# Kernel optimization log

Hardware: AMD Instinct MI355X
Metric: run time of the kernel (lower is better)

Reference implementation:

```python
import jax, jax.numpy as jnp
import numpy as np


def setup_inputs() -> dict:
    mesh = 2048
    N = mesh * mesh
    key = jax.random.key(0)
    k1, k2, k3, k4, k5 = jax.random.split(key, 5)
    theta = jax.random.normal(k1, (N - 1,), dtype=jnp.float32) * 1e-4
    phi = jax.random.normal(k2, (N - 1,), dtype=jnp.float32) * 1e-4
    psi = jax.random.normal(k3, (N - 1,), dtype=jnp.float32) * 1e-4
    state_re = jax.random.normal(k4, (N, 2, 1), dtype=jnp.float32)
    state_im = jax.random.normal(k5, (N, 2, 1), dtype=jnp.float32)
    # normalize spinors so |<s|s>| = 1 (physical states are normalized)
    norm = jnp.sqrt(jnp.sum(state_re**2 + state_im**2, axis=(1, 2), keepdims=True))
    state_re = state_re / norm
    state_im = state_im / norm
    return {"theta": theta, "phi": phi, "psi": psi,
            "state_re": state_re, "state_im": state_im}


def _deform(theta, phi, psi, state_re, state_im):
    # per-site SU(2) matrices, [N-1, 2, 2]
    ct, st = jnp.cos(theta), jnp.sin(theta)
    cp, sp = jnp.cos(phi), jnp.sin(phi)
    cq, sq = jnp.cos(psi), jnp.sin(psi)
    su_re = jnp.stack([jnp.stack([ct * cp, -st * cq], -1),
                       jnp.stack([st * cq, ct * cp], -1)], -2)  # [N-1,2,2]
    su_im = jnp.stack([jnp.stack([ct * sp, -st * sq], -1),
                       jnp.stack([-st * sq, -ct * sp], -1)], -2)
    d_re = jnp.einsum('nij,njk->nik', su_re, state_re[1:]) - \
           jnp.einsum('nij,njk->nik', su_im, state_im[1:])
    d_im = jnp.einsum('nij,njk->nik', su_re, state_im[1:]) + \
           jnp.einsum('nij,njk->nik', su_im, state_re[1:])
    def_re = jnp.concatenate([state_re[:1], d_re], axis=0)
    def_im = jnp.concatenate([state_im[:1], d_im], axis=0)
    return def_re, def_im


def _hs_distance(a_re, a_im, b_re, b_im):
    # Hilbert-Schmidt distance between 2-spinors, elementwise over leading dims
    rr = jnp.sum(a_re * b_re + a_im * b_im, axis=-1)
    ri = jnp.sum(a_re * b_im - a_im * b_re, axis=-1)
    return jnp.sqrt(jnp.abs(1.0 - rr**2 - ri**2))


def reference(theta, phi, psi, state_re, state_im):
    N = state_re.shape[0]
    mesh = int(np.sqrt(N))
    def_re, def_im = _deform(theta, phi, psi, state_re, state_im)
    # [mesh, mesh, 2] grids
    g_re = def_re.reshape(mesh, mesh, 2)
    g_im = def_im.reshape(mesh, mesh, 2)
    # v: neighbor at (i, j+1) with wrap; h: (i+1, j); d: (i+1, j+1)
    v = _hs_distance(g_re, g_im,
                     jnp.roll(g_re, -1, axis=1), jnp.roll(g_im, -1, axis=1))
    h = _hs_distance(g_re, g_im,
                     jnp.roll(g_re, -1, axis=0), jnp.roll(g_im, -1, axis=0))
    d = _hs_distance(g_re, g_im,
                     jnp.roll(jnp.roll(g_re, -1, axis=0), -1, axis=1),
                     jnp.roll(jnp.roll(g_im, -1, axis=0), -1, axis=1))
    return jnp.stack([v, h, d])  # [3, mesh, mesh]
```

## Files before the change

kernel.cpp:

```cpp
#include <hip/hip_runtime.h>
#include <math.h>

#define TILE  32
#define HALO  33
#define NHALO (HALO * HALO)
#define NGRP  9
#define NASSIGN (HALO * NGRP)
#define TPB   512

__device__ __forceinline__ float4 deform1(float th, float ph, float ps,
                                          float2 r, float2 im, bool origin) {
    float st, ct, sp, cp, sq, cq;
    __sincosf(th, &st, &ct);
    __sincosf(ph, &sp, &cp);
    __sincosf(ps, &sq, &cq);
    float a = ct * cp;
    float b = st * cq;
    float c = ct * sp;
    float d = st * sq;
    float4 d4;
    d4.x = a * r.x - b * r.y - c * im.x + d * im.y;
    d4.y = b * r.x + a * r.y + d * im.x + c * im.y;
    d4.z = a * im.x - b * im.y + c * r.x - d * r.y;
    d4.w = b * im.x + a * im.y - d * r.x - c * r.y;
    if (origin) d4 = make_float4(r.x, r.y, im.x, im.y);
    return d4;
}

__device__ __forceinline__ float hsdist(float4 A, float4 B) {
    float rr = A.x * B.x + A.y * B.y + A.z * B.z + A.w * B.w;
    float ri = A.x * B.z + A.y * B.w - A.z * B.x - A.w * B.y;
    return sqrtf(fabsf(1.0f - rr * rr - ri * ri));
}

__global__ __launch_bounds__(TPB, 4) void qwz_deform_dirichlet_kernel(
    const float* __restrict__ theta,
    const float* __restrict__ phi,
    const float* __restrict__ psi,
    const float2* __restrict__ sre,
    const float2* __restrict__ sim,
    float* __restrict__ out,
    int mesh)
{
    const int N = mesh * mesh;
    __shared__ float4 tile[NHALO];

    const int tid  = threadIdx.x;
    const int lane = tid & 63;
    const int bi = blockIdx.y * TILE;
    const int bj = blockIdx.x * TILE;

    if (tid < NASSIGN) {
        const int r = tid / NGRP;
        const int g = tid - r * NGRP;
        int gi = bi + r; if (gi >= mesh) gi -= mesh;
        const bool colwrap = (bj + 4 * g >= mesh);
        int gcol = bj + 4 * g; if (colwrap) gcol -= mesh;
        const int n0 = gi * mesh + gcol;

        float4 thq, phq, psq;
        if (n0 + 4 < N) {
            thq = *(const float4*)(theta + n0);
            phq = *(const float4*)(phi   + n0);
            psq = *(const float4*)(psi   + n0);
        } else {
            thq = make_float4(theta[n0], theta[n0 + 1], theta[n0 + 2], 0.f);
            phq = make_float4(phi[n0],   phi[n0 + 1],   phi[n0 + 2],   0.f);
            psq = make_float4(psi[n0],   psi[n0 + 1],   psi[n0 + 2],   0.f);
        }
        const float4 s01 = *(const float4*)((const float*)sre + 2 * n0);
        const float4 s23 = *(const float4*)((const float*)sre + 2 * n0 + 4);
        const float4 i01 = *(const float4*)((const float*)sim + 2 * n0);
        const float4 i23 = *(const float4*)((const float*)sim + 2 * n0 + 4);

        float thm = __shfl_up(thq.w, 1, 64);
        float phm = __shfl_up(phq.w, 1, 64);
        float psm = __shfl_up(psq.w, 1, 64);
        if (lane == 0 || g == 0 || colwrap) {
            int am = (n0 > 0) ? n0 - 1 : 0;
            thm = theta[am]; phm = phi[am]; psm = psi[am];
        }

        const int lbase = r * HALO + 4 * g;
        float4 d0 = deform1(thm, phm, psm,
                            make_float2(s01.x, s01.y), make_float2(i01.x, i01.y),
                            n0 == 0);
        tile[lbase] = d0;
        float4 d1 = deform1(thq.x, phq.x, psq.x,
                            make_float2(s01.z, s01.w), make_float2(i01.z, i01.w),
                            false);
        if (4 * g + 1 < HALO) tile[lbase + 1] = d1;
        float4 d2 = deform1(thq.y, phq.y, psq.y,
                            make_float2(s23.x, s23.y), make_float2(i23.x, i23.y),
                            false);
        if (4 * g + 2 < HALO) tile[lbase + 2] = d2;
        float4 d3 = deform1(thq.z, phq.z, psq.z,
                            make_float2(s23.z, s23.w), make_float2(i23.z, i23.w),
                            false);
        if (4 * g + 3 < HALO) tile[lbase + 3] = d3;
    }
    __syncthreads();

    const int trow = (tid >> 5) << 1;
    const int tcol = tid & 31;

    float4 A = tile[trow * HALO + tcol];
    float4 V = tile[trow * HALO + tcol + 1];
    int site = (bi + trow) * mesh + (bj + tcol);

#pragma unroll
    for (int k = 0; k < 2; ++k) {
        float4 H = tile[(trow + k + 1) * HALO + tcol];
        float4 D = tile[(trow + k + 1) * HALO + tcol + 1];

        float v = hsdist(A, V);
        float h = hsdist(A, H);
        float d = hsdist(A, D);

        __builtin_nontemporal_store(v, out + site);
        __builtin_nontemporal_store(h, out + N + site);
        __builtin_nontemporal_store(d, out + 2 * N + site);

        A = H; V = D;
        site += mesh;
    }
}

extern "C" void kernel_launch(void* const* d_in, const int* in_sizes, int n_in,
                              void* d_out, int out_size, void* d_ws, size_t ws_size,
                              hipStream_t stream) {
    const float* theta = (const float*)d_in[0];
    const float* phi   = (const float*)d_in[1];
    const float* psi   = (const float*)d_in[2];
    const float2* sre  = (const float2*)d_in[3];
    const float2* sim  = (const float2*)d_in[4];
    float* out = (float*)d_out;

    int N = in_sizes[0] + 1;
    int mesh = (int)(sqrt((double)N) + 0.5);

    dim3 grid(mesh / TILE, mesh / TILE);
    dim3 block(TPB);
    qwz_deform_dirichlet_kernel<<<grid, block, 0, stream>>>(
        theta, phi, psi, sre, sim, out, mesh);
}
```

Measured before the change: 165.1 us.

## Replace shared-memory halo tiles with register row-streaming and wave shuffles

Drops the 33x33 shared-memory tile and its barrier. Each thread now owns 4 consecutive columns across a strip of 4 rows, keeping deformed spinors in registers and software-pipelining the row loads against the deform step. Horizontal neighbours come from wave shuffles, with lane 63 loading one extra column, and outputs are written as 4-wide nontemporal vector stores. This cuts halo recompute from 33/32 to 5/4 rows and removes LDS traffic, but adds register pressure and still recomputes one row per strip.

```diff
diff --git a/kernel.cpp b/kernel.cpp
--- a/kernel.cpp
+++ b/kernel.cpp
@@ -1,12 +1,60 @@
 #include <hip/hip_runtime.h>
 #include <math.h>
 
-#define TILE  32
-#define HALO  33
-#define NHALO (HALO * HALO)
-#define NGRP  9
-#define NASSIGN (HALO * NGRP)
-#define TPB   512
+#define MESHW 1024
+#define RPB   4
+#define TPB   256
+
+typedef float vfloat4 __attribute__((ext_vector_type(4)));
+
+struct Raw {
+    float4 th, ph, ps;
+    float4 s01, s23;
+    float4 i01, i23;
+    float2 er, ei;
+    float  eth, eph, eps;
+    int    n0;
+    int    nx;
+};
+
+__device__ __forceinline__ void load_row(Raw& B, int r, int cj, int mesh, int N,
+    const float* __restrict__ theta, const float* __restrict__ phi,
+    const float* __restrict__ psi, const float2* __restrict__ sre,
+    const float2* __restrict__ sim, int lane)
+{
+    if (r >= mesh) r -= mesh;
+    const int n0 = r * mesh + cj;
+    B.n0 = n0;
+
+    if (n0 + 4 < N) {
+        B.th = *(const float4*)(theta + n0);
+        B.ph = *(const float4*)(phi   + n0);
+        B.ps = *(const float4*)(psi   + n0);
+    } else {
+        B.th = make_float4(theta[n0], theta[n0 + 1], theta[n0 + 2], 0.f);
+        B.ph = make_float4(phi[n0],   phi[n0 + 1],   phi[n0 + 2],   0.f);
+        B.ps = make_float4(psi[n0],   psi[n0 + 1],   psi[n0 + 2],   0.f);
+    }
+    const float4* sreq = (const float4*)sre;
+    const float4* simq = (const float4*)sim;
+    B.s01 = sreq[n0 >> 1];  B.s23 = sreq[(n0 >> 1) + 1];
+    B.i01 = simq[n0 >> 1];  B.i23 = simq[(n0 >> 1) + 1];
+
+    if (lane == 0) {
+        int a = (n0 > 0) ? n0 - 1 : 0;
+        B.eth = theta[a]; B.eph = phi[a]; B.eps = psi[a];
+    }
+    if (lane == 63) {
+        int jn = cj + 4; if (jn >= mesh) jn -= mesh;
+        int nx = r * mesh + jn;
+        B.nx = nx;
+        B.er = sre[nx]; B.ei = sim[nx];
+        if (jn == 0) {
+            int a = (nx > 0) ? nx - 1 : 0;
+            B.eth = theta[a]; B.eph = phi[a]; B.eps = psi[a];
+        }
+    }
+}
 
 __device__ __forceinline__ float4 deform1(float th, float ph, float ps,
                                           float2 r, float2 im, bool origin) {
@@ -27,10 +75,75 @@
     return d4;
 }
 
+__device__ __forceinline__ void deform_row(const Raw& B, float4 A[4],
+                                           float4& Aext, int lane)
+{
+    float thm = __shfl_up(B.th.w, 1, 64);
+    float phm = __shfl_up(B.ph.w, 1, 64);
+    float psm = __shfl_up(B.ps.w, 1, 64);
+    if (lane == 0) { thm = B.eth; phm = B.eph; psm = B.eps; }
+
+    A[0] = deform1(thm,    phm,    psm,
+                   make_float2(B.s01.x, B.s01.y), make_float2(B.i01.x, B.i01.y),
+                   B.n0 == 0);
+    A[1] = deform1(B.th.x, B.ph.x, B.ps.x,
+                   make_float2(B.s01.z, B.s01.w), make_float2(B.i01.z, B.i01.w),
+                   false);
+    A[2] = deform1(B.th.y, B.ph.y, B.ps.y,
+                   make_float2(B.s23.x, B.s23.y), make_float2(B.i23.x, B.i23.y),
+                   false);
+    A[3] = deform1(B.th.z, B.ph.z, B.ps.z,
+                   make_float2(B.s23.z, B.s23.w), make_float2(B.i23.z, B.i23.w),
+                   false);
+    if (lane == 63) {
+        float et = B.th.w, ep = B.ph.w, eq = B.ps.w;
+        if (B.nx != B.n0 + 4) { et = B.eth; ep = B.eph; eq = B.eps; }
+        Aext = deform1(et, ep, eq, B.er, B.ei, B.nx == 0);
+    }
+}
+
 __device__ __forceinline__ float hsdist(float4 A, float4 B) {
     float rr = A.x * B.x + A.y * B.y + A.z * B.z + A.w * B.w;
     float ri = A.x * B.z + A.y * B.w - A.z * B.x - A.w * B.y;
     return sqrtf(fabsf(1.0f - rr * rr - ri * ri));
+}
+
+__device__ __forceinline__ float4 shift_in(const float4 A0, const float4 Aext,
+                                           int lane)
+{
+    float4 n;
+    n.x = __shfl_down(A0.x, 1, 64);
+    n.y = __shfl_down(A0.y, 1, 64);
+    n.z = __shfl_down(A0.z, 1, 64);
+    n.w = __shfl_down(A0.w, 1, 64);
+    if (lane == 63) n = Aext;
+    return n;
+}
+
+__device__ __forceinline__ void nt_store4(float* p, float a, float b,
+                                          float c, float d)
+{
+    vfloat4 q = {a, b, c, d};
+    __builtin_nontemporal_store(q, (vfloat4*)p);
+}
+
+__device__ __forceinline__ void emit_row(const float4 A[4], const float4 Aext,
+    const float4 Bv[4], const float4 Bext, int row, int cj, int mesh, int N,
+    float* __restrict__ out, int lane)
+{
+    const float4 An = shift_in(A[0], Aext, lane);
+    const float4 Bn = shift_in(Bv[0], Bext, lane);
+
+    const int site = row * mesh + cj;
+    nt_store4(out + site,
+              hsdist(A[0], A[1]), hsdist(A[1], A[2]),
+              hsdist(A[2], A[3]), hsdist(A[3], An));
+    nt_store4(out + N + site,
+              hsdist(A[0], Bv[0]), hsdist(A[1], Bv[1]),
+              hsdist(A[2], Bv[2]), hsdist(A[3], Bv[3]));
+    nt_store4(out + 2 * N + site,
+              hsdist(A[0], Bv[1]), hsdist(A[1], Bv[2]),
+              hsdist(A[2], Bv[3]), hsdist(A[3], Bn));
 }
 
 __global__ __launch_bounds__(TPB, 4) void qwz_deform_dirichlet_kernel(
@@ -43,87 +156,35 @@
     int mesh)
 {
     const int N = mesh * mesh;
-    __shared__ float4 tile[NHALO];
-
     const int tid  = threadIdx.x;
     const int lane = tid & 63;
-    const int bi = blockIdx.y * TILE;
-    const int bj = blockIdx.x * TILE;
-
-    if (tid < NASSIGN) {
-        const int r = tid / NGRP;
-        const int g = tid - r * NGRP;
-        int gi = bi + r; if (gi >= mesh) gi -= mesh;
-        const bool colwrap = (bj + 4 * g >= mesh);
-        int gcol = bj + 4 * g; if (colwrap) gcol -= mesh;
-        const int n0 = gi * mesh + gcol;
-
-        float4 thq, phq, psq;
-        if (n0 + 4 < N) {
-            thq = *(const float4*)(theta + n0);
-            phq = *(const float4*)(phi   + n0);
-            psq = *(const float4*)(psi   + n0);
-        } else {
-            thq = make_float4(theta[n0], theta[n0 + 1], theta[n0 + 2], 0.f);
-            phq = make_float4(phi[n0],   phi[n0 + 1],   phi[n0 + 2],   0.f);
-            psq = make_float4(psi[n0],   psi[n0 + 1],   psi[n0 + 2],   0.f);
-        }
-        const float4 s01 = *(const float4*)((const float*)sre + 2 * n0);
-        const float4 s23 = *(const float4*)((const float*)sre + 2 * n0 + 4);
-        const float4 i01 = *(const float4*)((const float*)sim + 2 * n0);
-        const float4 i23 = *(const float4*)((const float*)sim + 2 * n0 + 4);
-
-        float thm = __shfl_up(thq.w, 1, 64);
-        float phm = __shfl_up(phq.w, 1, 64);
-        float psm = __shfl_up(psq.w, 1, 64);
-        if (lane == 0 || g == 0 || colwrap) {
-            int am = (n0 > 0) ? n0 - 1 : 0;
-            thm = theta[am]; phm = phi[am]; psm = psi[am];
-        }
-
-        const int lbase = r * HALO + 4 * g;
-        float4 d0 = deform1(thm, phm, psm,
-                            make_float2(s01.x, s01.y), make_float2(i01.x, i01.y),
-                            n0 == 0);
-        tile[lbase] = d0;
-        float4 d1 = deform1(thq.x, phq.x, psq.x,
-                            make_float2(s01.z, s01.w), make_float2(i01.z, i01.w),
-                            false);
-        if (4 * g + 1 < HALO) tile[lbase + 1] = d1;
-        float4 d2 = deform1(thq.y, phq.y, psq.y,
-                            make_float2(s23.x, s23.y), make_float2(i23.x, i23.y),
-                            false);
-        if (4 * g + 2 < HALO) tile[lbase + 2] = d2;
-        float4 d3 = deform1(thq.z, phq.z, psq.z,
-                            make_float2(s23.z, s23.w), make_float2(i23.z, i23.w),
-                            false);
-        if (4 * g + 3 < HALO) tile[lbase + 3] = d3;
-    }
-    __syncthreads();
-
-    const int trow = (tid >> 5) << 1;
-    const int tcol = tid & 31;
-
-    float4 A = tile[trow * HALO + tcol];
-    float4 V = tile[trow * HALO + tcol + 1];
-    int site = (bi + trow) * mesh + (bj + tcol);
-
-#pragma unroll
-    for (int k = 0; k < 2; ++k) {
-        float4 H = tile[(trow + k + 1) * HALO + tcol];
-        float4 D = tile[(trow + k + 1) * HALO + tcol + 1];
-
-        float v = hsdist(A, V);
-        float h = hsdist(A, H);
-        float d = hsdist(A, D);
-
-        __builtin_nontemporal_store(v, out + site);
-        __builtin_nontemporal_store(h, out + N + site);
-        __builtin_nontemporal_store(d, out + 2 * N + site);
-
-        A = H; V = D;
-        site += mesh;
-    }
+    const int cj = blockIdx.x * MESHW + 4 * tid;
+    const int r0 = blockIdx.y * RPB;
+
+    Raw ra, rb;
+    float4 A[4], B[4], Aext, Bext;
+
+    load_row(ra, r0,     cj, mesh, N, theta, phi, psi, sre, sim, lane);
+    load_row(rb, r0 + 1, cj, mesh, N, theta, phi, psi, sre, sim, lane);
+    deform_row(ra, A, Aext, lane);
+
+    load_row(ra, r0 + 2, cj, mesh, N, theta, phi, psi, sre, sim, lane);
+    deform_row(rb, B, Bext, lane);
+    emit_row(A, Aext, B, Bext, r0, cj, mesh, N, out, lane);
+    A[0] = B[0]; A[1] = B[1]; A[2] = B[2]; A[3] = B[3]; Aext = Bext;
+
+    load_row(rb, r0 + 3, cj, mesh, N, theta, phi, psi, sre, sim, lane);
+    deform_row(ra, B, Bext, lane);
+    emit_row(A, Aext, B, Bext, r0 + 1, cj, mesh, N, out, lane);
+    A[0] = B[0]; A[1] = B[1]; A[2] = B[2]; A[3] = B[3]; Aext = Bext;
+
+    load_row(ra, r0 + 4, cj, mesh, N, theta, phi, psi, sre, sim, lane);
+    deform_row(rb, B, Bext, lane);
+    emit_row(A, Aext, B, Bext, r0 + 2, cj, mesh, N, out, lane);
+    A[0] = B[0]; A[1] = B[1]; A[2] = B[2]; A[3] = B[3]; Aext = Bext;
+
+    deform_row(ra, B, Bext, lane);
+    emit_row(A, Aext, B, Bext, r0 + 3, cj, mesh, N, out, lane);
 }
 
 extern "C" void kernel_launch(void* const* d_in, const int* in_sizes, int n_in,
@@ -139,7 +200,7 @@
     int N = in_sizes[0] + 1;
     int mesh = (int)(sqrt((double)N) + 0.5);
 
-    dim3 grid(mesh / TILE, mesh / TILE);
+    dim3 grid(mesh / MESHW, mesh / RPB);
     dim3 block(TPB);
     qwz_deform_dirichlet_kernel<<<grid, block, 0, stream>>>(
         theta, phi, psi, sre, sim, out, mesh);
```

Result: no change. 166.5 us (+0.9%).
